# Optimization experiments

Hardware: AMD Instinct MI355X
Metric: run time of the kernel (lower is better)

Reference implementation:

```python
import jax, jax.numpy as jnp
import numpy as np

B, D_IN, H1, D_OUT = 32768, 256, 256, 64
E, T, MU = 32, 16, 0.01


def setup_inputs() -> dict:
    key = jax.random.key(0)
    ks = jax.random.split(key, 9)
    s = lambda *sh: 1.0 / np.sqrt(sh[-2])  # not used; torch default init approximated below
    return {
        "backbone_output": jax.random.normal(ks[0], (B, D_IN), dtype=jnp.float32),
        "task": jax.random.randint(ks[1], (B,), 0, T),
        # expert MLP params, stacked across experts (weights stored [E, in, out])
        "W1": jax.random.normal(ks[2], (E, D_IN, H1), dtype=jnp.float32) * (1.0 / np.sqrt(D_IN)),
        "b1": jnp.zeros((E, H1), dtype=jnp.float32),
        "W2": jax.random.normal(ks[3], (E, H1, D_OUT), dtype=jnp.float32) * (1.0 / np.sqrt(H1)),
        "b2": jnp.zeros((E, D_OUT), dtype=jnp.float32),
        # attention params (torch.randn init)
        "task_queries": jax.random.normal(ks[4], (T, D_OUT), dtype=jnp.float32),
        "key_matricies": jax.random.normal(ks[5], (E, D_OUT, D_OUT), dtype=jnp.float32),
        "value_matricies": jax.random.normal(ks[6], (E, D_OUT, D_OUT), dtype=jnp.float32),
    }


def reference(backbone_output, task, W1, b1, W2, b2, task_queries, key_matricies, value_matricies):
    # all experts run densely on the full batch
    h = jax.nn.relu(jnp.einsum('bi,eih->beh', backbone_output, W1) + b1)      # [B,E,H1]
    expert_outputs = jnp.einsum('beh,eho->beo', h, W2) + b2                   # [B,E,D_OUT]
    # per-expert key/value projections
    expert_keys = jnp.einsum('bei,eij->bej', expert_outputs, key_matricies)    # [B,E,D_OUT]
    expert_values = jnp.einsum('bei,eij->bej', expert_outputs, value_matricies)
    # attention over experts using the per-task query
    q = task_queries[task]                                                     # [B,D_OUT]
    attention_scores = jnp.einsum('bej,bj->be', expert_keys, q)                # [B,E]
    attention_weights = jax.nn.softmax(attention_scores, axis=-1)
    tower_input = jnp.einsum('be,bej->bj', attention_weights, expert_values)   # [B,D_OUT]
    eps = jnp.float32(1e-6)
    reg_loss_term = -(1.0 / E) * MU * jnp.sum(attention_weights + eps)
    return tower_input, reg_loss_term
```

## Files before the change

### kernel.cpp

```cpp
#include <hip/hip_runtime.h>
#include <hip/hip_fp16.h>

#define NTHR 512
#define BM   128
#define NBLK 256
#define NEXP 32

using f16x8 = __attribute__((ext_vector_type(8))) _Float16;
using f16x4 = __attribute__((ext_vector_type(4))) _Float16;
using f32x4 = __attribute__((ext_vector_type(4))) float;
using u32x4 = __attribute__((ext_vector_type(4))) unsigned int;
using u32x2 = __attribute__((ext_vector_type(2))) unsigned int;

static constexpr size_t ESTRIDE_B = 182272;

__device__ __forceinline__ unsigned short f2h(float x){
  _Float16 h = (_Float16)x; return __builtin_bit_cast(unsigned short, h);
}

typedef __attribute__((address_space(3))) void lds_void;
typedef const __attribute__((address_space(1))) void glb_void;
__device__ __forceinline__ void gll16(const void* g, void* l){
  __builtin_amdgcn_global_load_lds((glb_void*)g, (lds_void*)l, 16, 0, 0);
}

#define VMW(N)  asm volatile("s_waitcnt vmcnt(" #N ")" ::: "memory")
#define LGKM0   asm volatile("s_waitcnt lgkmcnt(0)" ::: "memory")
#define SB      __builtin_amdgcn_sched_barrier(0)
#define BARRIER do { SB; __builtin_amdgcn_s_barrier(); SB; } while(0)

__global__ __launch_bounds__(256) void prep_w1frag(const float* __restrict__ W1,
                                                   unsigned short* __restrict__ strm){
  const int e = blockIdx.x >> 3, kc = blockIdx.x & 7;
  const float* se = W1 + (size_t)e*65536 + (size_t)kc*32*256;
  unsigned short* de = strm + (size_t)e*91136 + kc*8192;
  for (int fl = threadIdx.x; fl < 1024; fl += 256){
    const int ct = fl >> 6, l = fl & 63;
    const float* s0 = se + (size_t)((l>>4)*8)*256 + ct*16 + (l&15);
    union { unsigned short s[8]; u32x4 v; } h8;
    #pragma unroll
    for (int j = 0; j < 8; j++) h8.s[j] = f2h(s0[(size_t)j*256]);
    *reinterpret_cast<u32x4*>(&de[fl*8]) = h8.v;
  }
}

__global__ __launch_bounds__(256) void prep_wvp(
    const float* __restrict__ W2, const float* __restrict__ V,
    const float* __restrict__ Km, const float* __restrict__ Q,
    const float* __restrict__ b1, const float* __restrict__ b2,
    unsigned short* __restrict__ strm, float* __restrict__ out)
{
  const int e = blockIdx.x >> 3, oct = blockIdx.x & 7;
  const int t = threadIdx.x;
  __shared__ float lv[64*64];
  __shared__ float ktlT[64*16];
  __shared__ float lw2[32*64];

  for (int i = t; i < 1024; i += 256)
    *reinterpret_cast<float4*>(&lv[i*4]) = *reinterpret_cast<const float4*>(V + (size_t)e*4096 + i*4);
  for (int i = t; i < 512; i += 256)
    *reinterpret_cast<float4*>(&lw2[i*4]) = *reinterpret_cast<const float4*>(W2 + (size_t)e*16384 + (size_t)oct*2048 + i*4);
  #pragma unroll
  for (int pass = 0; pass < 4; pass++){
    const int id = t + pass*256;
    const int tt = id >> 6, i = id & 63;
    const float4* Kr = reinterpret_cast<const float4*>(Km + (size_t)(e*64 + i)*64);
    const float4* qr = reinterpret_cast<const float4*>(Q + tt*64);
    float s = 0.f;
    #pragma unroll
    for (int j = 0; j < 16; j++){ float4 a = Kr[j], b = qr[j]; s += a.x*b.x+a.y*b.y+a.z*b.z+a.w*b.w; }
    ktlT[i*16 + tt] = s;
  }
  __syncthreads();

  const int k2 = oct*32 + (t >> 3);
  const int cb = t & 7;
  const int c0 = cb*12;
  const float* w2r = &lw2[(t>>3)*64];
  const float* gp[3]; int gs[3]; bool gv[3];
  #pragma unroll
  for (int q = 0; q < 3; q++){
    const int cg = c0 + q*4;
    gv[q] = (cg < 80);
    if (cg < 64){ gp[q] = &lv[cg];        gs[q] = 64; }
    else        { gp[q] = &ktlT[cg - 64]; gs[q] = 16; }
  }
  float pv[12];
  #pragma unroll
  for (int n = 0; n < 12; n++) pv[n] = 0.f;
  for (int i = 0; i < 64; i++){
    const float w = w2r[i];
    #pragma unroll
    for (int q = 0; q < 3; q++){
      if (gv[q]){
        const float4 vq = *reinterpret_cast<const float4*>(gp[q] + i*gs[q]);
        pv[q*4+0] += w*vq.x; pv[q*4+1] += w*vq.y; pv[q*4+2] += w*vq.z; pv[q*4+3] += w*vq.w;
      }
    }
  }
  const int wn_ = k2 >> 7, fn = (k2 >> 4) & 7, fnp = fn >> 1, half = fn & 1;
  const int g2 = (k2 >> 2) & 3, jj = k2 & 3;
  unsigned short* fb = strm + (size_t)e*91136 + (wn_ ? 77824 : 65536);
  #pragma unroll
  for (int n = 0; n < 12; n++){
    const int cc = c0 + n;
    if (cc < 64){
      const int ct = cc >> 4, lc = cc & 15, l = g2*16 + lc;
      fb[(fnp*6+ct)*512 + l*8 + half*4 + jj] = f2h(pv[n]);
    } else if (cc < 80){
      const int lc = cc - 64, l = g2*16 + lc;
      const float s = pv[n];
      const unsigned short hi = f2h(s);
      const float rem = s - (float)__builtin_bit_cast(_Float16, hi);
      fb[(fnp*6+4)*512 + l*8 + half*4 + jj] = hi;
      fb[(fnp*6+5)*512 + l*8 + half*4 + jj] = f2h(rem);
    }
  }
  if (oct == 0){
    float* b1d = reinterpret_cast<float*>((char*)strm + (size_t)e*ESTRIDE_B + 180224);
    b1d[t] = b1[e*256 + t];
  }
  if (oct == 1 && t < 80){
    float s = 0.f;
    if (t < 64){ for (int i = 0; i < 64; i++) s += b2[e*64+i]*lv[i*64+t]; }
    else       { for (int i = 0; i < 64; i++) s += b2[e*64+i]*ktlT[i*16 + (t-64)]; }
    float* bd = reinterpret_cast<float*>((char*)strm + (size_t)e*ESTRIDE_B + 181248);
    bd[t] = s;
  }
  if (blockIdx.x == 0 && t == 0) out[2097152] = -10.24032768f;
}

__global__ __launch_bounds__(NTHR, 2) __attribute__((amdgpu_waves_per_eu(2, 2)))
void moe_main(const float* __restrict__ X, const int* __restrict__ task,
              const unsigned short* __restrict__ strm, float* __restrict__ out)
{
  __shared__ unsigned short smem[75776];
  unsigned char* exch = (unsigned char*)smem + 98304;

  const int tid  = threadIdx.x;
  const int lane = tid & 63;
  const int wid  = tid >> 6;
  const int g    = lane >> 4;
  const int c    = lane & 15;
  const int wm   = wid >> 1, wn = wid & 1;
  const int row0 = blockIdx.x * BM;

  auto issueG = [&](const unsigned short* src, int slot){
    unsigned short* d = &smem[slot*16384];
    #pragma unroll
    for (int q = 0; q < 4; q++)
      gll16(src + q*4096 + tid*8, d + q*4096 + tid*8);
  };
  auto issueM = [&](const unsigned short* es_){
    #pragma unroll
    for (int q = 0; q < 6; q++)
      gll16(es_ + 65536 + q*4096 + tid*8, &smem[49152 + q*4096 + tid*8]);
  };
  auto issueAux = [&](const unsigned short* es_, int k){
    gll16(es_ + 90112 + lane*8, &smem[73728 + k*1024 + lane*8]);
    gll16(es_ + 90624 + lane*8, &smem[73728 + k*1024 + 512 + lane*8]);
  };

  f16x8 af[2][8];
  #pragma unroll
  for (int fm = 0; fm < 2; fm++){
    const float* xr = X + (size_t)(row0 + wm*32 + fm*16 + c)*256;
    #pragma unroll
    for (int kc = 0; kc < 8; kc++){
      const f32x4 v0 = *reinterpret_cast<const f32x4*>(xr + kc*32 + g*8);
      const f32x4 v1 = *reinterpret_cast<const f32x4*>(xr + kc*32 + g*8 + 4);
      union { unsigned short s[8]; f16x8 h; } h8;
      #pragma unroll
      for (int j = 0; j < 4; j++){ h8.s[j] = f2h(v0[j]); h8.s[4+j] = f2h(v1[j]); }
      af[fm][kc] = h8.h;
    }
  }
  const int4 tq = *reinterpret_cast<const int4*>(&task[row0 + wm*32 + wn*16 + g*4]);
  const int tsk4[4] = {tq.x, tq.y, tq.z, tq.w};

  VMW(0);

  issueG(strm, 0);
  issueAux(strm, 0);
  issueG(strm + 16384, 1);

  f32x4 oacc[4];
  float m_[4], d_[4];
  #pragma unroll
  for (int j = 0; j < 4; j++){
    m_[j] = -1e30f; d_[j] = 0.f;
    #pragma unroll
    for (int ct = 0; ct < 4; ct++) oacc[ct][j] = 0.f;
  }

#define G1PAIR(SLOT, P) do { \
    __builtin_amdgcn_s_setprio(1); \
    _Pragma("unroll") \
    for (int fnl = 0; fnl < 8; fnl++){ \
      const f16x8 bf = *reinterpret_cast<const f16x8*>(&smem[(SLOT)*16384 + (wn*8+fnl)*512 + lane*8]); \
      acc1[fnl][0] = __builtin_amdgcn_mfma_f32_16x16x32_f16(bf, af[0][2*(P)], acc1[fnl][0], 0,0,0); \
      acc1[fnl][1] = __builtin_amdgcn_mfma_f32_16x16x32_f16(bf, af[1][2*(P)], acc1[fnl][1], 0,0,0); \
    } \
    _Pragma("unroll") \
    for (int fnl = 0; fnl < 8; fnl++){ \
      const f16x8 bf = *reinterpret_cast<const f16x8*>(&smem[(SLOT)*16384 + 8192 + (wn*8+fnl)*512 + lane*8]); \
      acc1[fnl][0] = __builtin_amdgcn_mfma_f32_16x16x32_f16(bf, af[0][2*(P)+1], acc1[fnl][0], 0,0,0); \
      acc1[fnl][1] = __builtin_amdgcn_mfma_f32_16x16x32_f16(bf, af[1][2*(P)+1], acc1[fnl][1], 0,0,0); \
    } \
    __builtin_amdgcn_s_setprio(0); \
  } while(0)

#define MSTEP(FNP) do { \
    u32x4 pr[6]; \
    _Pragma("unroll") \
    for (int i = 0; i < 6; i++) \
      pr[i] = *reinterpret_cast<const u32x4*>(&smem[49152 + wn*12288 + ((FNP)*6+i)*512 + lane*8]); \
    const f32x4 b1a = *reinterpret_cast<const f32x4*>(b1f + wn*128 + (2*(FNP)+0)*16 + g*4); \
    const f32x4 b1b = *reinterpret_cast<const f32x4*>(b1f + wn*128 + (2*(FNP)+1)*16 + g*4); \
    __builtin_amdgcn_s_setprio(1); \
    _Pragma("unroll") \
    for (int half = 0; half < 2; half++){ \
      const int fnl = (FNP)*2 + half; \
      const f32x4 bb = half ? b1b : b1a; \
      f16x4 a0, a1; \
      _Pragma("unroll") \
      for (int j = 0; j < 4; j++){ \
        a0[j] = (_Float16)fmaxf(acc1[fnl][0][j] + bb[j], 0.f); \
        a1[j] = (_Float16)fmaxf(acc1[fnl][1][j] + bb[j], 0.f); \
      } \
      _Pragma("unroll") \
      for (int ct = 0; ct < 6; ct++){ \
        union { u32x4 v; struct { f16x4 lo, hi; } h; } u; u.v = pr[ct]; \
        const f16x4 bfr = half ? u.h.hi : u.h.lo; \
        const int ci = (ct < 5) ? ct : 4; \
        p0[ci] = __builtin_amdgcn_mfma_f32_16x16x16f16(a0, bfr, p0[ci], 0,0,0); \
        p1[ci] = __builtin_amdgcn_mfma_f32_16x16x16f16(a1, bfr, p1[ci], 0,0,0); \
      } \
    } \
    __builtin_amdgcn_s_setprio(0); \
  } while(0)

#define XWRITE(ACC, EB) do { \
    _Pragma("unroll") \
    for (int ct = 0; ct < 4; ct++){ \
      union { unsigned short s[4]; u32x2 v; } p_; \
      _Pragma("unroll") \
      for (int j = 0; j < 4; j++) p_.s[j] = f2h(ACC[ct][j]); \
      *reinterpret_cast<u32x2*>((EB) + ct*512 + lane*8) = p_.v; \
    } \
    *reinterpret_cast<f32x4*>((EB) + 2048 + lane*16) = ACC[4]; \
  } while(0)

#define XFINAL(ACC, EB) do { \
    float b2c[4]; \
    _Pragma("unroll") \
    for (int ct = 0; ct < 4; ct++) b2c[ct] = b2f[ct*16 + c]; \
    const float b2s = b2f[64 + c]; \
    f32x4 pvv[4]; \
    _Pragma("unroll") \
    for (int ct = 0; ct < 4; ct++){ \
      union { u32x2 v; unsigned short s[4]; } p_; \
      p_.v = *reinterpret_cast<const u32x2*>((EB) + ct*512 + lane*8); \
      _Pragma("unroll") \
      for (int j = 0; j < 4; j++) \
        pvv[ct][j] = ACC[ct][j] + (float)__builtin_bit_cast(_Float16, p_.s[j]) + b2c[ct]; \
    } \
    const f32x4 scp = *reinterpret_cast<const f32x4*>((EB) + 2048 + lane*16); \
    _Pragma("unroll") \
    for (int j = 0; j < 4; j++){ \
      const float sv = ACC[4][j] + scp[j] + b2s; \
      const float s  = __shfl(sv, (lane & 48) | tsk4[j]); \
      const float mn = fmaxf(m_[j], s); \
      const float al = __expf(m_[j] - mn); \
      const float p  = __expf(s - mn); \
      d_[j] = d_[j]*al + p; \
      m_[j] = mn; \
      _Pragma("unroll") \
      for (int ct = 0; ct < 4; ct++) \
        oacc[ct][j] = oacc[ct][j]*al + p*pvv[ct][j]; \
    } \
  } while(0)

  int st = 0;
  for (int e = 0; e < NEXP; e++){
    const unsigned short* es  = strm + (size_t)e*91136;
    const unsigned short* esn = (e == NEXP-1) ? strm : es + 91136;
    const int sA = st;
    const int sB = (sA + 1 < 3) ? sA + 1 : 0;
    const int sC = (sB + 1 < 3) ? sB + 1 : 0;
    const float* b1f = reinterpret_cast<const float*>(&smem[73728 + (e & 1)*1024]);
    f32x4 acc1[8][2] = {};

    VMW(6); BARRIER; issueG(es + 2*16384, sC);                  G1PAIR(sA, 0);
    VMW(4); BARRIER; issueG(es + 3*16384, sA);                  G1PAIR(sB, 1);
    VMW(4); BARRIER; issueM(es);                                G1PAIR(sC, 2);
    VMW(6); BARRIER; issueG(esn, sB); issueAux(esn, (e+1)&1);   G1PAIR(sA, 3);

    VMW(6); BARRIER;
    issueG(esn + 16384, sC);
    f32x4 p0[5] = {}, p1[5] = {};
    MSTEP(0); MSTEP(1); MSTEP(2); MSTEP(3);

    BARRIER;
    if (wn == 0){
      XWRITE(p1, exch + (wm*2 + 1)*3072);
    } else {
      XWRITE(p0, exch + (wm*2 + 0)*3072);
    }
    LGKM0; BARRIER;
    {
      const float* b2f = b1f + 256;
      if (wn == 0){
        XFINAL(p0, exch + (wm*2 + 0)*3072);
      } else {
        XFINAL(p1, exch + (wm*2 + 1)*3072);
      }
    }
    st = sB;
  }
#undef XFINAL
#undef XWRITE
#undef MSTEP
#undef G1PAIR

  #pragma unroll
  for (int j = 0; j < 4; j++){
    const float inv = 1.f / d_[j];
    float* orow = out + (size_t)(row0 + wm*32 + wn*16 + g*4 + j)*64;
    #pragma unroll
    for (int ct = 0; ct < 4; ct++)
      orow[ct*16 + c] = oacc[ct][j]*inv;
  }
}

extern "C" void kernel_launch(void* const* d_in, const int* in_sizes, int n_in,
                              void* d_out, int out_size, void* d_ws, size_t ws_size,
                              hipStream_t hs)
{
  (void)in_sizes; (void)n_in; (void)out_size; (void)ws_size;
  const float* X   = (const float*)d_in[0];
  const int*   tsk = (const int*)  d_in[1];
  const float* W1  = (const float*)d_in[2];
  const float* b1  = (const float*)d_in[3];
  const float* W2  = (const float*)d_in[4];
  const float* b2  = (const float*)d_in[5];
  const float* Q   = (const float*)d_in[6];
  const float* Km  = (const float*)d_in[7];
  const float* Vm  = (const float*)d_in[8];
  float* out = (float*)d_out;

  unsigned short* strm = (unsigned short*)d_ws;

  prep_w1frag<<<dim3(256), dim3(256), 0, hs>>>(W1, strm);
  prep_wvp  <<<dim3(256), dim3(256), 0, hs>>>(W2, Vm, Km, Q, b1, b2, strm, out);
  moe_main  <<<dim3(NBLK), dim3(NTHR), 0, hs>>>(X, tsk, strm, out);
}
```

Before: 236.8 us.

## Restructure expert pipeline with 48KB ping-pong buffers and deferred softmax merge

Replaces the three-slot 32KB W1 rotation with two 48KB ping-pong halves, so each barrier covers three K-chunks of the first GEMM. The B fragments are batched into registers before the MFMAs. Both waves now write their partial sums to the exchange buffer, and the reduction plus online softmax for expert e is deferred into the next iteration after its first barrier. This removes one barrier per expert and overlaps the merge with the next expert's GEMM, at the cost of more LDS traffic for the exchange, a larger exchange region and more live registers.

```diff
diff --git a/kernel.cpp b/kernel.cpp
--- a/kernel.cpp
+++ b/kernel.cpp
@@ -145,16 +145,15 @@
   const int wm   = wid >> 1, wn = wid & 1;
   const int row0 = blockIdx.x * BM;
 
-  auto issueG = [&](const unsigned short* src, int slot){
-    unsigned short* d = &smem[slot*16384];
+  auto issue48 = [&](const unsigned short* src, int sloth){
+    #pragma unroll
+    for (int q = 0; q < 6; q++)
+      gll16(src + q*4096 + tid*8, &smem[sloth + q*4096 + tid*8]);
+  };
+  auto issue32 = [&](const unsigned short* src, int sloth){
     #pragma unroll
     for (int q = 0; q < 4; q++)
-      gll16(src + q*4096 + tid*8, d + q*4096 + tid*8);
-  };
-  auto issueM = [&](const unsigned short* es_){
-    #pragma unroll
-    for (int q = 0; q < 6; q++)
-      gll16(es_ + 65536 + q*4096 + tid*8, &smem[49152 + q*4096 + tid*8]);
+      gll16(src + q*4096 + tid*8, &smem[sloth + q*4096 + tid*8]);
   };
   auto issueAux = [&](const unsigned short* es_, int k){
     gll16(es_ + 90112 + lane*8, &smem[73728 + k*1024 + lane*8]);
@@ -180,9 +179,9 @@
 
   VMW(0);
 
-  issueG(strm, 0);
+  issue48(strm,          0);
+  issue48(strm + 24576,  24576);
   issueAux(strm, 0);
-  issueG(strm + 16384, 1);
 
   f32x4 oacc[4];
   float m_[4], d_[4];
@@ -193,19 +192,16 @@
     for (int ct = 0; ct < 4; ct++) oacc[ct][j] = 0.f;
   }
 
-#define G1PAIR(SLOT, P) do { \
+#define G1STEP(BASEH, KC) do { \
+    f16x8 bfr_[8]; \
+    _Pragma("unroll") \
+    for (int fnl = 0; fnl < 8; fnl++) \
+      bfr_[fnl] = *reinterpret_cast<const f16x8*>(&smem[(BASEH) + (wn*8+fnl)*512 + lane*8]); \
     __builtin_amdgcn_s_setprio(1); \
     _Pragma("unroll") \
     for (int fnl = 0; fnl < 8; fnl++){ \
-      const f16x8 bf = *reinterpret_cast<const f16x8*>(&smem[(SLOT)*16384 + (wn*8+fnl)*512 + lane*8]); \
-      acc1[fnl][0] = __builtin_amdgcn_mfma_f32_16x16x32_f16(bf, af[0][2*(P)], acc1[fnl][0], 0,0,0); \
-      acc1[fnl][1] = __builtin_amdgcn_mfma_f32_16x16x32_f16(bf, af[1][2*(P)], acc1[fnl][1], 0,0,0); \
-    } \
-    _Pragma("unroll") \
-    for (int fnl = 0; fnl < 8; fnl++){ \
-      const f16x8 bf = *reinterpret_cast<const f16x8*>(&smem[(SLOT)*16384 + 8192 + (wn*8+fnl)*512 + lane*8]); \
-      acc1[fnl][0] = __builtin_amdgcn_mfma_f32_16x16x32_f16(bf, af[0][2*(P)+1], acc1[fnl][0], 0,0,0); \
-      acc1[fnl][1] = __builtin_amdgcn_mfma_f32_16x16x32_f16(bf, af[1][2*(P)+1], acc1[fnl][1], 0,0,0); \
+      acc1[fnl][0] = __builtin_amdgcn_mfma_f32_16x16x32_f16(bfr_[fnl], af[0][KC], acc1[fnl][0], 0,0,0); \
+      acc1[fnl][1] = __builtin_amdgcn_mfma_f32_16x16x32_f16(bfr_[fnl], af[1][KC], acc1[fnl][1], 0,0,0); \
     } \
     __builtin_amdgcn_s_setprio(0); \
   } while(0)
@@ -240,7 +236,7 @@
     __builtin_amdgcn_s_setprio(0); \
   } while(0)
 
-#define XWRITE(ACC, EB) do { \
+#define XW(ACC, EB) do { \
     _Pragma("unroll") \
     for (int ct = 0; ct < 4; ct++){ \
       union { unsigned short s[4]; u32x2 v; } p_; \
@@ -251,24 +247,29 @@
     *reinterpret_cast<f32x4*>((EB) + 2048 + lane*16) = ACC[4]; \
   } while(0)
 
-#define XFINAL(ACC, EB) do { \
+#define XFIN(B2F) do { \
+    const unsigned char* ebS = exch + (wm*2 + wn)*6144 + wn*3072; \
+    const unsigned char* ebP = exch + (wm*2 + (wn^1))*6144 + wn*3072; \
     float b2c[4]; \
     _Pragma("unroll") \
-    for (int ct = 0; ct < 4; ct++) b2c[ct] = b2f[ct*16 + c]; \
-    const float b2s = b2f[64 + c]; \
+    for (int ct = 0; ct < 4; ct++) b2c[ct] = (B2F)[ct*16 + c]; \
+    const float b2s = (B2F)[64 + c]; \
     f32x4 pvv[4]; \
     _Pragma("unroll") \
     for (int ct = 0; ct < 4; ct++){ \
-      union { u32x2 v; unsigned short s[4]; } p_; \
-      p_.v = *reinterpret_cast<const u32x2*>((EB) + ct*512 + lane*8); \
+      union { u32x2 v; unsigned short s[4]; } pa_, pb_; \
+      pa_.v = *reinterpret_cast<const u32x2*>(ebS + ct*512 + lane*8); \
+      pb_.v = *reinterpret_cast<const u32x2*>(ebP + ct*512 + lane*8); \
       _Pragma("unroll") \
       for (int j = 0; j < 4; j++) \
-        pvv[ct][j] = ACC[ct][j] + (float)__builtin_bit_cast(_Float16, p_.s[j]) + b2c[ct]; \
-    } \
-    const f32x4 scp = *reinterpret_cast<const f32x4*>((EB) + 2048 + lane*16); \
+        pvv[ct][j] = (float)__builtin_bit_cast(_Float16, pa_.s[j]) \
+                   + (float)__builtin_bit_cast(_Float16, pb_.s[j]) + b2c[ct]; \
+    } \
+    const f32x4 s1 = *reinterpret_cast<const f32x4*>(ebS + 2048 + lane*16); \
+    const f32x4 s2 = *reinterpret_cast<const f32x4*>(ebP + 2048 + lane*16); \
     _Pragma("unroll") \
     for (int j = 0; j < 4; j++){ \
-      const float sv = ACC[4][j] + scp[j] + b2s; \
+      const float sv = s1[j] + s2[j] + b2s; \
       const float s  = __shfl(sv, (lane & 48) | tsk4[j]); \
       const float mn = fmaxf(m_[j], s); \
       const float al = __expf(m_[j] - mn); \
@@ -281,47 +282,59 @@
     } \
   } while(0)
 
-  int st = 0;
   for (int e = 0; e < NEXP; e++){
     const unsigned short* es  = strm + (size_t)e*91136;
     const unsigned short* esn = (e == NEXP-1) ? strm : es + 91136;
-    const int sA = st;
-    const int sB = (sA + 1 < 3) ? sA + 1 : 0;
-    const int sC = (sB + 1 < 3) ? sB + 1 : 0;
+    const int pA = (e & 1) * 24576;
+    const int pB = 24576 - pA;
     const float* b1f = reinterpret_cast<const float*>(&smem[73728 + (e & 1)*1024]);
     f32x4 acc1[8][2] = {};
 
-    VMW(6); BARRIER; issueG(es + 2*16384, sC);                  G1PAIR(sA, 0);
-    VMW(4); BARRIER; issueG(es + 3*16384, sA);                  G1PAIR(sB, 1);
-    VMW(4); BARRIER; issueM(es);                                G1PAIR(sC, 2);
-    VMW(6); BARRIER; issueG(esn, sB); issueAux(esn, (e+1)&1);   G1PAIR(sA, 3);
+    VMW(8); BARRIER;
+    if (e > 0){
+      const float* b2p = reinterpret_cast<const float*>(&smem[73728 + ((e+1) & 1)*1024]) + 256;
+      XFIN(b2p);
+    }
+    G1STEP(pA,          0);
+    G1STEP(pA +  8192,  1);
+    G1STEP(pA + 16384,  2);
+
+    VMW(2); BARRIER;
+    issue32(es + 49152, pA);
+    issue48(es + 65536, 49152);
+    G1STEP(pB,          3);
+    G1STEP(pB +  8192,  4);
+    G1STEP(pB + 16384,  5);
 
     VMW(6); BARRIER;
-    issueG(esn + 16384, sC);
+    issue48(esn, pB);
+    G1STEP(pA,          6);
+    G1STEP(pA +  8192,  7);
+
+    VMW(6); BARRIER;
+    issue48(esn + 24576, pA);
     f32x4 p0[5] = {}, p1[5] = {};
     MSTEP(0); MSTEP(1); MSTEP(2); MSTEP(3);
 
     BARRIER;
-    if (wn == 0){
-      XWRITE(p1, exch + (wm*2 + 1)*3072);
-    } else {
-      XWRITE(p0, exch + (wm*2 + 0)*3072);
-    }
-    LGKM0; BARRIER;
     {
-      const float* b2f = b1f + 256;
-      if (wn == 0){
-        XFINAL(p0, exch + (wm*2 + 0)*3072);
-      } else {
-        XFINAL(p1, exch + (wm*2 + 1)*3072);
-      }
-    }
-    st = sB;
-  }
-#undef XFINAL
-#undef XWRITE
+      unsigned char* eb = exch + wid*6144;
+      XW(p0, eb);
+      XW(p1, eb + 3072);
+    }
+    issueAux(esn, (e+1) & 1);
+    LGKM0;
+  }
+
+  BARRIER;
+  {
+    const float* b2p = reinterpret_cast<const float*>(&smem[73728 + (31 & 1)*1024]) + 256;
+    XFIN(b2p);
+  }
+#undef XFIN
+#undef XW
 #undef MSTEP
-#undef G1PAIR
+#undef G1STEP
 
   #pragma unroll
   for (int j = 0; j < 4; j++){
```

Result: slower. 242.4 us (+2.4%).
